# Optimization experiments

Measured on AMD Instinct MI355X. Metric: run time of the kernel, lower is better.

## Reference

```python
import jax, jax.numpy as jnp
import numpy as np

N_HEAD = 16
RMS_EPS = 1.1920928955078125e-07  # torch float32 finfo eps (F.rms_norm default)


def _apply_rotary(x, cos, sin):
    # x: [B,T,H,D], cos/sin: [1,T,1,D/2]
    d = x.shape[-1] // 2
    x1, x2 = x[..., :d], x[..., d:]
    return jnp.concatenate([x1 * cos + x2 * sin, -x1 * sin + x2 * cos], axis=-1)


def _rms_norm(x):
    var = jnp.mean(jnp.square(x), axis=-1, keepdims=True)
    return x * jax.lax.rsqrt(var + RMS_EPS)


def setup_inputs() -> dict:
    key = jax.random.key(0)
    ks = jax.random.split(key, 5)
    B, T, C, H = 2, 2048, 1024, N_HEAD
    D = C // H
    x = jax.random.normal(ks[0], (B, T, C), dtype=jnp.float32)
    cos = jax.random.uniform(ks[1], (1, T, 1, D // 2), dtype=jnp.float32)
    sin = jax.random.uniform(ks[2], (1, T, 1, D // 2), dtype=jnp.float32)
    kv_w = jax.random.normal(ks[3], (C, C), dtype=jnp.float32) * (C ** -0.5)
    proj_w = jax.random.normal(ks[4], (C, C), dtype=jnp.float32) * (C ** -0.5)
    return {"x": x, "cos": cos, "sin": sin, "kv_w": kv_w, "proj_w": proj_w, "window_left": 1024}


def reference(x, cos, sin, kv_w, proj_w, window_left):
    B, T, C = x.shape
    H = N_HEAD
    D = C // H
    scale = D ** -0.5

    q = x.reshape(B, T, H, D)                       # no Q projection
    kv = (x @ kv_w.T).reshape(B, T, H, D)           # tied K=V projection

    q = _rms_norm(_apply_rotary(q, cos, sin))
    kv = _rms_norm(_apply_rotary(kv, cos, sin))

    # scores: [B,H,T,T]
    scores = jnp.einsum('bqhd,bkhd->bhqk', q, kv) * scale

    pos = jnp.arange(T)
    dist = pos[:, None] - pos[None, :]              # query_pos - key_pos
    allowed = (dist >= 0) & (dist <= window_left)   # causal + sliding window
    scores = jnp.where(allowed[None, None], scores, -jnp.inf)

    attn = jax.nn.softmax(scores, axis=-1)
    out = jnp.einsum('bhqk,bkhd->bqhd', attn, kv).reshape(B, T, C)
    return out @ proj_w.T
```

## Files before the change

### kernel.cpp

```cpp
#include <hip/hip_runtime.h>
#include <hip/hip_bf16.h>

using u16 = unsigned short;
typedef __attribute__((ext_vector_type(8))) short short8v;
typedef __attribute__((ext_vector_type(4))) float f32x4;

#define MFMA16(a, b, c) __builtin_amdgcn_mfma_f32_16x16x32_bf16((a), (b), (c), 0, 0, 0)

static __device__ __forceinline__ u16 f2bf(float x) {
  __hip_bfloat16 h = __float2bfloat16(x);
  return __builtin_bit_cast(u16, h);
}

__global__ __launch_bounds__(256) void cast_f32_bf16(const float* __restrict__ s,
                                                     u16* __restrict__ d, int n) {
  int i = (blockIdx.x * 256 + threadIdx.x) * 4;
  if (i >= n) return;
  float4 v = *reinterpret_cast<const float4*>(s + i);
  ushort4 o;
  o.x = f2bf(v.x); o.y = f2bf(v.y); o.z = f2bf(v.z); o.w = f2bf(v.w);
  *reinterpret_cast<ushort4*>(d + i) = o;
}

__global__ __launch_bounds__(256) void gemm_bt(const u16* __restrict__ A,
                                               const u16* __restrict__ Bt,
                                               float* __restrict__ C,
                                               int M, int N, int K) {
  __shared__ u16 As[128][40];
  __shared__ u16 Bs[128][40];
  int bm = blockIdx.x, bn = blockIdx.y;
  int tid = threadIdx.x;
  int l = tid & 63, lr = l & 15, lg = l >> 4;
  int wid = tid >> 6, wr = wid >> 1, wc = wid & 1;

  int row0 = tid >> 2, seg = tid & 3;
  int row1 = row0 + 64;
  const u16* Ab = A + (size_t)(bm * 128) * K + seg * 8;
  const u16* Bb = Bt + (size_t)(bn * 128) * K + seg * 8;

  f32x4 acc[4][4];
#pragma unroll
  for (int m = 0; m < 4; m++)
#pragma unroll
    for (int n = 0; n < 4; n++) acc[m][n] = (f32x4){0.f, 0.f, 0.f, 0.f};

  short8v ra0 = *reinterpret_cast<const short8v*>(Ab + (size_t)row0 * K);
  short8v ra1 = *reinterpret_cast<const short8v*>(Ab + (size_t)row1 * K);
  short8v rb0 = *reinterpret_cast<const short8v*>(Bb + (size_t)row0 * K);
  short8v rb1 = *reinterpret_cast<const short8v*>(Bb + (size_t)row1 * K);

  for (int k0 = 0; k0 < K; k0 += 32) {
    __syncthreads();
    *reinterpret_cast<short8v*>(&As[row0][seg * 8]) = ra0;
    *reinterpret_cast<short8v*>(&As[row1][seg * 8]) = ra1;
    *reinterpret_cast<short8v*>(&Bs[row0][seg * 8]) = rb0;
    *reinterpret_cast<short8v*>(&Bs[row1][seg * 8]) = rb1;
    __syncthreads();
    if (k0 + 32 < K) {
      ra0 = *reinterpret_cast<const short8v*>(Ab + (size_t)row0 * K + k0 + 32);
      ra1 = *reinterpret_cast<const short8v*>(Ab + (size_t)row1 * K + k0 + 32);
      rb0 = *reinterpret_cast<const short8v*>(Bb + (size_t)row0 * K + k0 + 32);
      rb1 = *reinterpret_cast<const short8v*>(Bb + (size_t)row1 * K + k0 + 32);
    }

    short8v af[4], bfr[4];
#pragma unroll
    for (int m = 0; m < 4; m++)
      af[m] = *reinterpret_cast<const short8v*>(&As[wr * 64 + m * 16 + lr][lg * 8]);
#pragma unroll
    for (int n = 0; n < 4; n++)
      bfr[n] = *reinterpret_cast<const short8v*>(&Bs[wc * 64 + n * 16 + lr][lg * 8]);
#pragma unroll
    for (int m = 0; m < 4; m++)
#pragma unroll
      for (int n = 0; n < 4; n++) acc[m][n] = MFMA16(af[m], bfr[n], acc[m][n]);
  }

#pragma unroll
  for (int m = 0; m < 4; m++)
#pragma unroll
    for (int n = 0; n < 4; n++)
#pragma unroll
      for (int r = 0; r < 4; r++) {
        int row = bm * 128 + wr * 64 + m * 16 + lg * 4 + r;
        int col = bn * 128 + wc * 64 + n * 16 + lr;
        C[(size_t)row * N + col] = acc[m][n][r];
      }
}

__global__ __launch_bounds__(256) void rope_rms(const float* __restrict__ src,
                                                u16* __restrict__ dst,
                                                const float* __restrict__ cosp,
                                                const float* __restrict__ sinp) {
  int R = blockIdx.x * 4 + (threadIdx.x >> 6);
  int l = threadIdx.x & 63;
  int h = R & 15;
  int bt = R >> 4;
  int t = bt & 2047, b = bt >> 11;

  float v = src[((size_t)R << 6) + l];
  float p = __shfl_xor(v, 32);
  float c = cosp[(t << 5) + (l & 31)];
  float s = sinp[(t << 5) + (l & 31)];
  float r = v * c + ((l < 32) ? p * s : -p * s);
  float sq = r * r;
  sq += __shfl_xor(sq, 32);
  sq += __shfl_xor(sq, 16);
  sq += __shfl_xor(sq, 8);
  sq += __shfl_xor(sq, 4);
  sq += __shfl_xor(sq, 2);
  sq += __shfl_xor(sq, 1);
  float inv = rsqrtf(sq * (1.0f / 64.0f) + 1.1920928955078125e-07f);
  dst[((((size_t)b * 16 + h) * 2048 + t) << 6) + l] = f2bf(r * inv);
}

__global__ __launch_bounds__(256) void transpose_td(const u16* __restrict__ src,
                                                    u16* __restrict__ dst) {
  __shared__ u16 Ld[64][72];
  int t0 = blockIdx.x << 6, bh = blockIdx.y;
  int tid = threadIdx.x;
#pragma unroll
  for (int i = 0; i < 2; i++) {
    int c = tid + i * 256, tr = c >> 3, sg = c & 7;
    *reinterpret_cast<short8v*>(&Ld[tr][sg * 8]) =
        *reinterpret_cast<const short8v*>(src + ((size_t)bh * 2048 + t0 + tr) * 64 + sg * 8);
  }
  __syncthreads();
#pragma unroll
  for (int i = 0; i < 2; i++) {
    int c = tid + i * 256, dr = c >> 3, sg = c & 7;
    short8v v;
#pragma unroll
    for (int j = 0; j < 8; j++) v[j] = (short)Ld[sg * 8 + j][dr];
    *reinterpret_cast<short8v*>(dst + ((size_t)bh * 64 + dr) * 2048 + t0 + sg * 8) = v;
  }
}

__global__ __launch_bounds__(256) void attn_swa(const u16* __restrict__ Q,
                                                const u16* __restrict__ KV,
                                                const u16* __restrict__ KVt,
                                                u16* __restrict__ O,
                                                const int* __restrict__ winp) {
  const int T = 2048;
  int bid = blockIdx.x;
  int bh = bid & 31;
  int qi = 31 - (bid >> 5);
  int q0 = qi << 6;
  int b = bh >> 4, h = bh & 15;
  int W = *winp;
  int tid = threadIdx.x;
  int wid = tid >> 6, l = tid & 63, lr = l & 15, lg = l >> 4;

  __shared__ u16 Kl[64][72];
  __shared__ u16 Vt[64][72];
  __shared__ u16 Pl[4][16][72];

  const u16* Qb = Q + (((size_t)bh * T + q0 + wid * 16 + lr) << 6);
  short8v aq0 = *reinterpret_cast<const short8v*>(Qb + lg * 8);
  short8v aq1 = *reinterpret_cast<const short8v*>(Qb + 32 + lg * 8);

  float m_run[4], l_run[4];
  f32x4 oacc[4];
#pragma unroll
  for (int r = 0; r < 4; r++) { m_run[r] = -1e30f; l_run[r] = 0.f; }
#pragma unroll
  for (int dt = 0; dt < 4; dt++) oacc[dt] = (f32x4){0.f, 0.f, 0.f, 0.f};

  int lo = q0 - W;
  if (lo < 0) lo = 0;
  lo &= ~63;

  const u16* KVbh  = KV + (((size_t)bh * T) << 6);
  const u16* KVtbh = KVt + ((size_t)bh << 6) * T;
  int r8 = tid >> 3, sg = tid & 7;

  short8v vK0 = *reinterpret_cast<const short8v*>(KVbh + ((size_t)(lo + r8) << 6) + sg * 8);
  short8v vK1 = *reinterpret_cast<const short8v*>(KVbh + ((size_t)(lo + r8 + 32) << 6) + sg * 8);
  short8v vV0 = *reinterpret_cast<const short8v*>(KVtbh + (size_t)r8 * T + lo + sg * 8);
  short8v vV1 = *reinterpret_cast<const short8v*>(KVtbh + (size_t)(r8 + 32) * T + lo + sg * 8);

  for (int kt = lo; kt <= q0; kt += 64) {
    __syncthreads();
    *reinterpret_cast<short8v*>(&Kl[r8][sg * 8]) = vK0;
    *reinterpret_cast<short8v*>(&Kl[r8 + 32][sg * 8]) = vK1;
    *reinterpret_cast<short8v*>(&Vt[r8][sg * 8]) = vV0;
    *reinterpret_cast<short8v*>(&Vt[r8 + 32][sg * 8]) = vV1;
    __syncthreads();
    if (kt < q0) {
      vK0 = *reinterpret_cast<const short8v*>(KVbh + ((size_t)(kt + 64 + r8) << 6) + sg * 8);
      vK1 = *reinterpret_cast<const short8v*>(KVbh + ((size_t)(kt + 64 + r8 + 32) << 6) + sg * 8);
      vV0 = *reinterpret_cast<const short8v*>(KVtbh + (size_t)r8 * T + kt + 64 + sg * 8);
      vV1 = *reinterpret_cast<const short8v*>(KVtbh + (size_t)(r8 + 32) * T + kt + 64 + sg * 8);
    }

    f32x4 s[4];
#pragma unroll
    for (int nt = 0; nt < 4; nt++) {
      s[nt] = (f32x4){0.f, 0.f, 0.f, 0.f};
      short8v b0 = *reinterpret_cast<const short8v*>(&Kl[nt * 16 + lr][lg * 8]);
      s[nt] = MFMA16(aq0, b0, s[nt]);
      short8v b1 = *reinterpret_cast<const short8v*>(&Kl[nt * 16 + lr][32 + lg * 8]);
      s[nt] = MFMA16(aq1, b1, s[nt]);
    }

#pragma unroll
    for (int r = 0; r < 4; r++) {
      int t = q0 + wid * 16 + lg * 4 + r;
      float sv[4];
      float mt = -3e38f;
#pragma unroll
      for (int nt = 0; nt < 4; nt++) {
        int k = kt + nt * 16 + lr;
        float val = ((k <= t) && (t - k <= W)) ? s[nt][r] * 0.125f : -3e38f;
        sv[nt] = val;
        mt = fmaxf(mt, val);
      }
      mt = fmaxf(mt, __shfl_xor(mt, 1));
      mt = fmaxf(mt, __shfl_xor(mt, 2));
      mt = fmaxf(mt, __shfl_xor(mt, 4));
      mt = fmaxf(mt, __shfl_xor(mt, 8));
      float mn = fmaxf(m_run[r], mt);
      float al = __expf(m_run[r] - mn);
      m_run[r] = mn;
      float rs = 0.f;
#pragma unroll
      for (int nt = 0; nt < 4; nt++) {
        float pv = __expf(sv[nt] - mn);
        rs += pv;
        Pl[wid][lg * 4 + r][nt * 16 + lr] = f2bf(pv);
      }
      rs += __shfl_xor(rs, 1);
      rs += __shfl_xor(rs, 2);
      rs += __shfl_xor(rs, 4);
      rs += __shfl_xor(rs, 8);
      l_run[r] = l_run[r] * al + rs;
#pragma unroll
      for (int dt = 0; dt < 4; dt++) oacc[dt][r] *= al;
    }

    short8v ap0 = *reinterpret_cast<const short8v*>(&Pl[wid][lr][lg * 8]);
    short8v ap1 = *reinterpret_cast<const short8v*>(&Pl[wid][lr][32 + lg * 8]);
#pragma unroll
    for (int dt = 0; dt < 4; dt++) {
      short8v v0 = *reinterpret_cast<const short8v*>(&Vt[dt * 16 + lr][lg * 8]);
      oacc[dt] = MFMA16(ap0, v0, oacc[dt]);
      short8v v1 = *reinterpret_cast<const short8v*>(&Vt[dt * 16 + lr][32 + lg * 8]);
      oacc[dt] = MFMA16(ap1, v1, oacc[dt]);
    }
  }

#pragma unroll
  for (int r = 0; r < 4; r++) {
    int t = q0 + wid * 16 + lg * 4 + r;
    float inv = 1.f / l_run[r];
#pragma unroll
    for (int dt = 0; dt < 4; dt++) {
      O[(((size_t)b * T + t) << 10) + (h << 6) + dt * 16 + lr] = f2bf(oacc[dt][r] * inv);
    }
  }
}

extern "C" void kernel_launch(void* const* d_in, const int* in_sizes, int n_in,
                              void* d_out, int out_size, void* d_ws, size_t ws_size,
                              hipStream_t stream) {
  (void)in_sizes; (void)n_in; (void)out_size; (void)ws_size;
  const float* x    = (const float*)d_in[0];
  const float* cosp = (const float*)d_in[1];
  const float* sinp = (const float*)d_in[2];
  const float* kvw  = (const float*)d_in[3];
  const float* pw   = (const float*)d_in[4];
  const int*   win  = (const int*)d_in[5];

  char* w = (char*)d_ws;
  u16*   xbf   = (u16*)(w);
  u16*   kvwbf = (u16*)(w + (8u << 20));
  u16*   pwbf  = (u16*)(w + (10u << 20));
  float* kvf   = (float*)(w + (12u << 20));
  u16*   kvt   = (u16*)(w + (12u << 20));
  u16*   aout  = (u16*)(w + (20u << 20));
  u16*   kvbf  = (u16*)(w + (28u << 20));
  u16*   qbf   = xbf;

  cast_f32_bf16<<<4096, 256, 0, stream>>>(x, xbf, 4194304);
  cast_f32_bf16<<<1024, 256, 0, stream>>>(kvw, kvwbf, 1048576);
  cast_f32_bf16<<<1024, 256, 0, stream>>>(pw, pwbf, 1048576);

  gemm_bt<<<dim3(32, 8), 256, 0, stream>>>(xbf, kvwbf, kvf, 4096, 1024, 1024);

  rope_rms<<<16384, 256, 0, stream>>>(x, qbf, cosp, sinp);
  rope_rms<<<16384, 256, 0, stream>>>(kvf, kvbf, cosp, sinp);

  transpose_td<<<dim3(32, 32), 256, 0, stream>>>(kvbf, kvt);

  attn_swa<<<1024, 256, 0, stream>>>(qbf, kvbf, kvt, aout, win);

  gemm_bt<<<dim3(32, 8), 256, 0, stream>>>(aout, pwbf, (float*)d_out, 4096, 1024, 1024);
}
```

Baseline: 205.1 us.

## Use direct global-to-LDS loads in GEMM and streamline attention softmax

The GEMM drops to 64x128 tiles with twice as many blocks and loads tiles straight into LDS through global_load_lds, replacing the register-staged prefetch. The attention kernel folds the softmax scale and log2(e) into Q, switches to exp2f, skips mask evaluation for interior tiles, and computes row sums with an MFMA against a ones vector instead of shuffle reductions. These aim to cut VALU work in attention and improve GEMM occupancy. The cost is losing the GEMM's load/compute overlap, an unpadded LDS layout that may cause bank conflicts, and row sums taken from bf16-rounded probabilities.

```diff
diff --git a/kernel.cpp b/kernel.cpp
--- a/kernel.cpp
+++ b/kernel.cpp
@@ -6,6 +6,10 @@
 typedef __attribute__((ext_vector_type(4))) float f32x4;
 
 #define MFMA16(a, b, c) __builtin_amdgcn_mfma_f32_16x16x32_bf16((a), (b), (c), 0, 0, 0)
+
+#define GLOAD16(g, l) __builtin_amdgcn_global_load_lds(                       \
+    (const __attribute__((address_space(1))) void*)(const void*)(g),          \
+    (__attribute__((address_space(3))) void*)(void*)(l), 16, 0, 0)
 
 static __device__ __forceinline__ u16 f2bf(float x) {
   __hip_bfloat16 h = __float2bfloat16(x);
@@ -26,63 +30,54 @@
                                                const u16* __restrict__ Bt,
                                                float* __restrict__ C,
                                                int M, int N, int K) {
-  __shared__ u16 As[128][40];
-  __shared__ u16 Bs[128][40];
+  __shared__ u16 As[64 * 32];
+  __shared__ u16 Bs[128 * 32];
   int bm = blockIdx.x, bn = blockIdx.y;
   int tid = threadIdx.x;
-  int l = tid & 63, lr = l & 15, lg = l >> 4;
-  int wid = tid >> 6, wr = wid >> 1, wc = wid & 1;
-
-  int row0 = tid >> 2, seg = tid & 3;
-  int row1 = row0 + 64;
-  const u16* Ab = A + (size_t)(bm * 128) * K + seg * 8;
-  const u16* Bb = Bt + (size_t)(bn * 128) * K + seg * 8;
-
-  f32x4 acc[4][4];
-#pragma unroll
-  for (int m = 0; m < 4; m++)
+  int wid = tid >> 6, l = tid & 63, lr = l & 15, lg = l >> 4;
+  int wr = wid >> 1, wc = wid & 1;
+
+  int srow = l >> 2, scol = (l & 3) * 8;
+  const u16* Ag  = A  + (size_t)(bm * 64 + wid * 16 + srow) * K + scol;
+  const u16* Bg0 = Bt + (size_t)(bn * 128 + wid * 32 + srow) * K + scol;
+  const u16* Bg1 = Bg0 + (size_t)16 * K;
+  u16* Asb  = &As[wid * 512];
+  u16* Bsb0 = &Bs[wid * 1024];
+  u16* Bsb1 = &Bs[wid * 1024 + 512];
+
+  f32x4 acc[2][4];
+#pragma unroll
+  for (int m = 0; m < 2; m++)
 #pragma unroll
     for (int n = 0; n < 4; n++) acc[m][n] = (f32x4){0.f, 0.f, 0.f, 0.f};
-
-  short8v ra0 = *reinterpret_cast<const short8v*>(Ab + (size_t)row0 * K);
-  short8v ra1 = *reinterpret_cast<const short8v*>(Ab + (size_t)row1 * K);
-  short8v rb0 = *reinterpret_cast<const short8v*>(Bb + (size_t)row0 * K);
-  short8v rb1 = *reinterpret_cast<const short8v*>(Bb + (size_t)row1 * K);
 
   for (int k0 = 0; k0 < K; k0 += 32) {
     __syncthreads();
-    *reinterpret_cast<short8v*>(&As[row0][seg * 8]) = ra0;
-    *reinterpret_cast<short8v*>(&As[row1][seg * 8]) = ra1;
-    *reinterpret_cast<short8v*>(&Bs[row0][seg * 8]) = rb0;
-    *reinterpret_cast<short8v*>(&Bs[row1][seg * 8]) = rb1;
+    GLOAD16(Ag + k0, Asb);
+    GLOAD16(Bg0 + k0, Bsb0);
+    GLOAD16(Bg1 + k0, Bsb1);
     __syncthreads();
-    if (k0 + 32 < K) {
-      ra0 = *reinterpret_cast<const short8v*>(Ab + (size_t)row0 * K + k0 + 32);
-      ra1 = *reinterpret_cast<const short8v*>(Ab + (size_t)row1 * K + k0 + 32);
-      rb0 = *reinterpret_cast<const short8v*>(Bb + (size_t)row0 * K + k0 + 32);
-      rb1 = *reinterpret_cast<const short8v*>(Bb + (size_t)row1 * K + k0 + 32);
-    }
-
-    short8v af[4], bfr[4];
-#pragma unroll
-    for (int m = 0; m < 4; m++)
-      af[m] = *reinterpret_cast<const short8v*>(&As[wr * 64 + m * 16 + lr][lg * 8]);
+
+    short8v af[2], bfr[4];
+#pragma unroll
+    for (int m = 0; m < 2; m++)
+      af[m] = *reinterpret_cast<const short8v*>(&As[(wr * 32 + m * 16 + lr) * 32 + lg * 8]);
 #pragma unroll
     for (int n = 0; n < 4; n++)
-      bfr[n] = *reinterpret_cast<const short8v*>(&Bs[wc * 64 + n * 16 + lr][lg * 8]);
-#pragma unroll
-    for (int m = 0; m < 4; m++)
+      bfr[n] = *reinterpret_cast<const short8v*>(&Bs[(wc * 64 + n * 16 + lr) * 32 + lg * 8]);
+#pragma unroll
+    for (int m = 0; m < 2; m++)
 #pragma unroll
       for (int n = 0; n < 4; n++) acc[m][n] = MFMA16(af[m], bfr[n], acc[m][n]);
   }
 
 #pragma unroll
-  for (int m = 0; m < 4; m++)
+  for (int m = 0; m < 2; m++)
 #pragma unroll
     for (int n = 0; n < 4; n++)
 #pragma unroll
       for (int r = 0; r < 4; r++) {
-        int row = bm * 128 + wr * 64 + m * 16 + lg * 4 + r;
+        int row = bm * 64 + wr * 32 + m * 16 + lg * 4 + r;
         int col = bn * 128 + wc * 64 + n * 16 + lr;
         C[(size_t)row * N + col] = acc[m][n][r];
       }
@@ -91,7 +86,8 @@
 __global__ __launch_bounds__(256) void rope_rms(const float* __restrict__ src,
                                                 u16* __restrict__ dst,
                                                 const float* __restrict__ cosp,
-                                                const float* __restrict__ sinp) {
+                                                const float* __restrict__ sinp,
+                                                float scale) {
   int R = blockIdx.x * 4 + (threadIdx.x >> 6);
   int l = threadIdx.x & 63;
   int h = R & 15;
@@ -110,7 +106,7 @@
   sq += __shfl_xor(sq, 4);
   sq += __shfl_xor(sq, 2);
   sq += __shfl_xor(sq, 1);
-  float inv = rsqrtf(sq * (1.0f / 64.0f) + 1.1920928955078125e-07f);
+  float inv = rsqrtf(sq * (1.0f / 64.0f) + 1.1920928955078125e-07f) * scale;
   dst[((((size_t)b * 16 + h) * 2048 + t) << 6) + l] = f2bf(r * inv);
 }
 
@@ -159,6 +155,9 @@
   short8v aq0 = *reinterpret_cast<const short8v*>(Qb + lg * 8);
   short8v aq1 = *reinterpret_cast<const short8v*>(Qb + 32 + lg * 8);
 
+  const short one_bf = (short)0x3F80;
+  short8v vones = {one_bf, one_bf, one_bf, one_bf, one_bf, one_bf, one_bf, one_bf};
+
   float m_run[4], l_run[4];
   f32x4 oacc[4];
 #pragma unroll
@@ -203,43 +202,48 @@
       s[nt] = MFMA16(aq1, b1, s[nt]);
     }
 
+    bool edge = (kt + 63 > q0 + wid * 16) || ((q0 - kt) + wid * 16 + 15 > W);
+
+    float al4[4];
 #pragma unroll
     for (int r = 0; r < 4; r++) {
-      int t = q0 + wid * 16 + lg * 4 + r;
-      float sv[4];
-      float mt = -3e38f;
-#pragma unroll
-      for (int nt = 0; nt < 4; nt++) {
-        int k = kt + nt * 16 + lr;
-        float val = ((k <= t) && (t - k <= W)) ? s[nt][r] * 0.125f : -3e38f;
-        sv[nt] = val;
-        mt = fmaxf(mt, val);
+      float sv[4], mt;
+      if (edge) {
+        int t = q0 + wid * 16 + lg * 4 + r;
+        mt = -3e38f;
+#pragma unroll
+        for (int nt = 0; nt < 4; nt++) {
+          int k = kt + nt * 16 + lr;
+          float val = ((k <= t) && (t - k <= W)) ? s[nt][r] : -3e38f;
+          sv[nt] = val;
+          mt = fmaxf(mt, val);
+        }
+      } else {
+#pragma unroll
+        for (int nt = 0; nt < 4; nt++) sv[nt] = s[nt][r];
+        mt = fmaxf(fmaxf(sv[0], sv[1]), fmaxf(sv[2], sv[3]));
       }
       mt = fmaxf(mt, __shfl_xor(mt, 1));
       mt = fmaxf(mt, __shfl_xor(mt, 2));
       mt = fmaxf(mt, __shfl_xor(mt, 4));
       mt = fmaxf(mt, __shfl_xor(mt, 8));
       float mn = fmaxf(m_run[r], mt);
-      float al = __expf(m_run[r] - mn);
+      float al = exp2f(m_run[r] - mn);
       m_run[r] = mn;
-      float rs = 0.f;
+      al4[r] = al;
 #pragma unroll
       for (int nt = 0; nt < 4; nt++) {
-        float pv = __expf(sv[nt] - mn);
-        rs += pv;
-        Pl[wid][lg * 4 + r][nt * 16 + lr] = f2bf(pv);
+        Pl[wid][lg * 4 + r][nt * 16 + lr] = f2bf(exp2f(sv[nt] - mn));
       }
-      rs += __shfl_xor(rs, 1);
-      rs += __shfl_xor(rs, 2);
-      rs += __shfl_xor(rs, 4);
-      rs += __shfl_xor(rs, 8);
-      l_run[r] = l_run[r] * al + rs;
 #pragma unroll
       for (int dt = 0; dt < 4; dt++) oacc[dt][r] *= al;
     }
 
     short8v ap0 = *reinterpret_cast<const short8v*>(&Pl[wid][lr][lg * 8]);
     short8v ap1 = *reinterpret_cast<const short8v*>(&Pl[wid][lr][32 + lg * 8]);
+    f32x4 psum = (f32x4){0.f, 0.f, 0.f, 0.f};
+    psum = MFMA16(ap0, vones, psum);
+    psum = MFMA16(ap1, vones, psum);
 #pragma unroll
     for (int dt = 0; dt < 4; dt++) {
       short8v v0 = *reinterpret_cast<const short8v*>(&Vt[dt * 16 + lr][lg * 8]);
@@ -247,6 +251,8 @@
       short8v v1 = *reinterpret_cast<const short8v*>(&Vt[dt * 16 + lr][32 + lg * 8]);
       oacc[dt] = MFMA16(ap1, v1, oacc[dt]);
     }
+#pragma unroll
+    for (int r = 0; r < 4; r++) l_run[r] = l_run[r] * al4[r] + psum[r];
   }
 
 #pragma unroll
@@ -285,14 +291,14 @@
   cast_f32_bf16<<<1024, 256, 0, stream>>>(kvw, kvwbf, 1048576);
   cast_f32_bf16<<<1024, 256, 0, stream>>>(pw, pwbf, 1048576);
 
-  gemm_bt<<<dim3(32, 8), 256, 0, stream>>>(xbf, kvwbf, kvf, 4096, 1024, 1024);
-
-  rope_rms<<<16384, 256, 0, stream>>>(x, qbf, cosp, sinp);
-  rope_rms<<<16384, 256, 0, stream>>>(kvf, kvbf, cosp, sinp);
+  gemm_bt<<<dim3(64, 8), 256, 0, stream>>>(xbf, kvwbf, kvf, 4096, 1024, 1024);
+
+  rope_rms<<<16384, 256, 0, stream>>>(x, qbf, cosp, sinp, 0.18033688011112042f);
+  rope_rms<<<16384, 256, 0, stream>>>(kvf, kvbf, cosp, sinp, 1.0f);
 
   transpose_td<<<dim3(32, 32), 256, 0, stream>>>(kvbf, kvt);
 
   attn_swa<<<1024, 256, 0, stream>>>(qbf, kvbf, kvt, aout, win);
 
-  gemm_bt<<<dim3(32, 8), 256, 0, stream>>>(aout, pwbf, (float*)d_out, 4096, 1024, 1024);
-}
+  gemm_bt<<<dim3(64, 8), 256, 0, stream>>>(aout, pwbf, (float*)d_out, 4096, 1024, 1024);
+}
```

New measurement: 203.9 us. Within noise of the previous version (-0.6%).
